# Optimization experiments

Measured on AMD Instinct MI355X. Metric: run time of the kernel, lower is better.

## Reference

```python
import jax, jax.numpy as jnp
import numpy as np

NUM_HEADS = 16


def setup_inputs() -> dict:
    key = jax.random.key(0)
    ks = jax.random.split(key, 6)
    B, S, D = 2, 2048, 1024
    x = jax.random.normal(ks[0], (B, S, D), dtype=jnp.float32)
    # Linear weights stored as [d_in, d_out] so forward is x @ W (qkv_bias=False)
    scale = 1.0 / np.sqrt(D)
    Wq = jax.random.normal(ks[1], (D, D), dtype=jnp.float32) * scale
    Wk = jax.random.normal(ks[2], (D, D), dtype=jnp.float32) * scale
    Wv = jax.random.normal(ks[3], (D, D), dtype=jnp.float32) * scale
    Wo = jax.random.normal(ks[4], (D, D), dtype=jnp.float32) * scale
    bo = jax.random.normal(ks[5], (D,), dtype=jnp.float32) * 0.01
    return {"x": x, "Wq": Wq, "Wk": Wk, "Wv": Wv, "Wo": Wo, "bo": bo}


def reference(x, Wq, Wk, Wv, Wo, bo):
    B, S, D = x.shape
    H = NUM_HEADS
    hd = D // H

    def split_heads(t):  # [B,S,D] -> [B,H,S,hd]
        return t.reshape(B, S, H, hd).transpose(0, 2, 1, 3)

    q = split_heads(x @ Wq)
    k = split_heads(x @ Wk)
    v = split_heads(x @ Wv)

    # full score matrix [B,H,S,S]
    scores = jnp.einsum('bhsd,bhtd->bhst', q, k)
    causal = jnp.triu(jnp.ones((S, S), dtype=bool), k=1)
    scores = jnp.where(causal, -jnp.inf, scores)
    attn = jax.nn.softmax(scores * (hd ** -0.5), axis=-1)
    # dropout p=0.0 -> identity
    out = jnp.einsum('bhst,bhtd->bhsd', attn, v)
    out = out.transpose(0, 2, 1, 3).reshape(B, S, D)
    return out @ Wo + bo
```

## Files before the change

### kernel.cpp

```cpp
#include <hip/hip_runtime.h>

typedef unsigned short ushort_t;
typedef unsigned int uint_t;
typedef __attribute__((ext_vector_type(8))) short short8;
typedef __attribute__((ext_vector_type(4))) float floatx4;

#define S_LEN 2048
#define D_DIM 1024
#define H_NUM 16
#define HD 64
#define GBUF (128 * 32)

__device__ __forceinline__ float bf2f(ushort_t u) {
    union { uint_t i; float f; } c; c.i = ((uint_t)u) << 16; return c.f;
}
__device__ __forceinline__ ushort_t f2bf(float f) {
    union { float f; uint_t i; } c; c.f = f;
    uint_t r = c.i + 0x7fffu + ((c.i >> 16) & 1u);
    return (ushort_t)(r >> 16);
}

__device__ __forceinline__ void g2l16(const ushort_t* g, ushort_t* l) {
    __builtin_amdgcn_global_load_lds(
        (const __attribute__((address_space(1))) void*)g,
        (__attribute__((address_space(3))) void*)l, 16, 0, 0);
}

__global__ __launch_bounds__(256, 4) void cast_x_kernel(
        const float* __restrict__ in, ushort_t* __restrict__ out) {
    const int idx = (blockIdx.x * 256 + threadIdx.x) * 4;
    const float4 v = *(const float4*)(in + idx);
    ushort4 o;
    o.x = f2bf(v.x); o.y = f2bf(v.y); o.z = f2bf(v.z); o.w = f2bf(v.w);
    *(ushort4*)(out + idx) = o;
}

__global__ __launch_bounds__(256, 2) void transpose4_kernel(
        const float* __restrict__ W0, const float* __restrict__ W1,
        const float* __restrict__ W2, const float* __restrict__ W3,
        ushort_t* __restrict__ T0, ushort_t* __restrict__ T1,
        ushort_t* __restrict__ T2, ushort_t* __restrict__ T3) {
    const int z = blockIdx.z;
    const float* in  = (z == 0) ? W0 : (z == 1) ? W1 : (z == 2) ? W2 : W3;
    ushort_t*    out = (z == 0) ? T0 : (z == 1) ? T1 : (z == 2) ? T2 : T3;
    __shared__ __align__(16) ushort_t t[64][65];
    const int r0 = blockIdx.y * 64, c0 = blockIdx.x * 64;
    const int tr = threadIdx.x >> 4;
    const int tc = (threadIdx.x & 15) * 4;
#pragma unroll
    for (int i = 0; i < 4; ++i) {
        const int row = tr + i * 16;
        const float4 v = *(const float4*)(in + (size_t)(r0 + row) * D_DIM + c0 + tc);
        t[row][tc + 0] = f2bf(v.x); t[row][tc + 1] = f2bf(v.y);
        t[row][tc + 2] = f2bf(v.z); t[row][tc + 3] = f2bf(v.w);
    }
    __syncthreads();
#pragma unroll
    for (int i = 0; i < 4; ++i) {
        const int n = tr + i * 16;
        ushort4 v;
        v.x = t[tc + 0][n]; v.y = t[tc + 1][n];
        v.z = t[tc + 2][n]; v.w = t[tc + 3][n];
        *(ushort4*)(out + (size_t)(c0 + n) * D_DIM + r0 + tc) = v;
    }
}

__device__ __forceinline__ void gemm_tile(
        const ushort_t* __restrict__ A, const ushort_t* __restrict__ BT,
        const int m0, const int n0,
        ushort_t* As, ushort_t* Bs, floatx4 acc[4][4]) {
    const int tid  = threadIdx.x;
    const int w    = tid >> 6;
    const int wm   = (w >> 1) * 64;
    const int wn   = (w & 1) * 64;
    const int lrow = tid & 15;
    const int kq   = ((tid & 63) >> 4) * 8;

    const int flat0 = tid * 8;
    const int flat1 = (256 + tid) * 8;
    const int row0 = flat0 >> 5, kk0 = flat0 & 31;
    const int row1 = flat1 >> 5, kk1 = flat1 & 31;

    const ushort_t* ga0 = A  + (size_t)(m0 + row0) * D_DIM + kk0;
    const ushort_t* gb0 = BT + (size_t)(n0 + row0) * D_DIM + kk0;
    const ushort_t* ga1 = A  + (size_t)(m0 + row1) * D_DIM + kk1;
    const ushort_t* gb1 = BT + (size_t)(n0 + row1) * D_DIM + kk1;

    g2l16(ga0, As + flat0);
    g2l16(gb0, Bs + flat0);
    g2l16(ga1, As + flat1);
    g2l16(gb1, Bs + flat1);
    asm volatile("s_waitcnt vmcnt(0)" ::: "memory");
    __syncthreads();

    int cur = 0;
    for (int k0 = 0; k0 < D_DIM; k0 += 32) {
        const ushort_t* Ac = As + cur * GBUF;
        const ushort_t* Bc = Bs + cur * GBUF;
        short8 av[4], bv[4];
#pragma unroll
        for (int i = 0; i < 4; ++i)
            av[i] = *(const short8*)(Ac + (wm + i * 16 + lrow) * 32 + kq);
#pragma unroll
        for (int j = 0; j < 4; ++j)
            bv[j] = *(const short8*)(Bc + (wn + j * 16 + lrow) * 32 + kq);

        if (k0 + 32 < D_DIM) {
            ushort_t* An = As + (cur ^ 1) * GBUF;
            ushort_t* Bn = Bs + (cur ^ 1) * GBUF;
            g2l16(ga0 + k0 + 32, An + flat0);
            g2l16(gb0 + k0 + 32, Bn + flat0);
            g2l16(ga1 + k0 + 32, An + flat1);
            g2l16(gb1 + k0 + 32, Bn + flat1);
        }

#pragma unroll
        for (int i = 0; i < 4; ++i)
#pragma unroll
            for (int j = 0; j < 4; ++j)
                acc[i][j] = __builtin_amdgcn_mfma_f32_16x16x32_bf16(
                    av[i], bv[j], acc[i][j], 0, 0, 0);

        asm volatile("s_waitcnt vmcnt(0)" ::: "memory");
        __syncthreads();
        cur ^= 1;
    }
}

__global__ __launch_bounds__(256, 2) void gemm_qkv_kernel(
        const ushort_t* __restrict__ A,
        const ushort_t* __restrict__ WqT, const ushort_t* __restrict__ WkT,
        const ushort_t* __restrict__ WvT,
        ushort_t* __restrict__ Qo, ushort_t* __restrict__ Ko,
        ushort_t* __restrict__ Vo) {
    const ushort_t* BT = (blockIdx.z == 0) ? WqT : (blockIdx.z == 1) ? WkT : WvT;
    ushort_t* C        = (blockIdx.z == 0) ? Qo  : (blockIdx.z == 1) ? Ko  : Vo;
    const float sc     = (blockIdx.z == 0) ? 0.125f : 1.0f;
    __shared__ __align__(16) ushort_t As[2 * GBUF];
    __shared__ __align__(16) ushort_t Bs[2 * GBUF];
    const int m0 = blockIdx.y * 128, n0 = blockIdx.x * 128;

    floatx4 acc[4][4] = {};
    gemm_tile(A, BT, m0, n0, As, Bs, acc);

    const int tid = threadIdx.x;
    const int w = tid >> 6, wm = (w >> 1) * 64, wn = (w & 1) * 64;
    const int lrow = tid & 15;
    const int rquad = ((tid & 63) >> 4) * 4;
#pragma unroll
    for (int i = 0; i < 4; ++i) {
        const int mbase = m0 + wm + i * 16 + rquad;
#pragma unroll
        for (int j = 0; j < 4; ++j) {
            const int gn = n0 + wn + j * 16 + lrow;
#pragma unroll
            for (int r = 0; r < 4; ++r)
                C[(size_t)(mbase + r) * D_DIM + gn] = f2bf(acc[i][j][r] * sc);
        }
    }
}

__global__ __launch_bounds__(256, 2) void gemm_out_kernel(
        const ushort_t* __restrict__ A, const ushort_t* __restrict__ WoT,
        const float* __restrict__ bias, float* __restrict__ C) {
    __shared__ __align__(16) ushort_t As[2 * GBUF];
    __shared__ __align__(16) ushort_t Bs[2 * GBUF];
    const int m0 = blockIdx.y * 128, n0 = blockIdx.x * 128;

    floatx4 acc[4][4] = {};
    gemm_tile(A, WoT, m0, n0, As, Bs, acc);

    const int tid = threadIdx.x;
    const int w = tid >> 6, wm = (w >> 1) * 64, wn = (w & 1) * 64;
    const int lrow = tid & 15;
    const int rquad = ((tid & 63) >> 4) * 4;
#pragma unroll
    for (int i = 0; i < 4; ++i) {
        const int mbase = m0 + wm + i * 16 + rquad;
#pragma unroll
        for (int j = 0; j < 4; ++j) {
            const int gn = n0 + wn + j * 16 + lrow;
            const float badd = bias[gn];
#pragma unroll
            for (int r = 0; r < 4; ++r)
                C[(size_t)(mbase + r) * D_DIM + gn] = acc[i][j][r] + badd;
        }
    }
}

__global__ __launch_bounds__(256, 4) void attn_mfma_kernel(
        const ushort_t* __restrict__ Q, const ushort_t* __restrict__ K,
        const ushort_t* __restrict__ V, ushort_t* __restrict__ O) {
    __shared__ __align__(16) ushort_t Ks[64 * 64];
    __shared__ __align__(16) ushort_t Vt[64 * 64];
    __shared__ __align__(16) ushort_t Ps[4][16 * 64];

    const int bh  = blockIdx.x;
    const int b   = bh >> 4, h = bh & 15;
    const int g   = blockIdx.y & 7;
    const int p   = blockIdx.y >> 3;
    const int qt  = (p == 0) ? g : (p == 1) ? (15 - g)
                  : (p == 2) ? (16 + g) : (31 - g);
    const int q0  = qt * 64;
    const int tid = threadIdx.x;
    const int wq  = tid >> 6;
    const int lane = tid & 63;
    const int col  = lane & 15;
    const int quad = lane >> 4;
    const int c7 = col & 7;
    const int qw0  = q0 + wq * 16;
    const size_t rowbase = (size_t)b * S_LEN;
    const int ch0 = h * HD;

    const int skey = tid >> 2;
    const int schk = tid & 3;
    const int vkp = tid & 31;
    const int vdc = tid >> 5;

    short8 aq[2];
#pragma unroll
    for (int kc = 0; kc < 2; ++kc)
        aq[kc] = *(const short8*)(Q + (rowbase + qw0 + col) * D_DIM
                                    + ch0 + kc * 32 + quad * 8);

    floatx4 oacc[4] = {};
    float mrun[4], lrun[4];
#pragma unroll
    for (int r = 0; r < 4; ++r) { mrun[r] = -1e30f; lrun[r] = 0.0f; }

    const int ntiles = qt + 1;

    short8 krA, krB, vrA, vrB;
    {
        const ushort_t* kg = K + (rowbase + skey) * D_DIM + ch0 + schk * 16;
        krA = *(const short8*)(kg);
        krB = *(const short8*)(kg + 8);
        const ushort_t* vg = V + (rowbase + 2 * vkp) * D_DIM + ch0 + vdc * 8;
        vrA = *(const short8*)(vg);
        vrB = *(const short8*)(vg + D_DIM);
    }

    for (int t = 0; t < ntiles; ++t) {
        const int kb = t * 64;
        __syncthreads();
        {
            const int sw = skey & 7;
            *(short8*)(Ks + skey * 64 + (((2 * schk) ^ sw) << 3)) = krA;
            *(short8*)(Ks + skey * 64 + (((2 * schk + 1) ^ sw) << 3)) = krB;
        }
#pragma unroll
        for (int e = 0; e < 8; ++e) {
            const int d = vdc * 8 + e;
            const uint_t pk = (uint_t)(ushort_t)vrA[e] | ((uint_t)(ushort_t)vrB[e] << 16);
            *(uint_t*)(Vt + d * 64 + ((2 * vkp) ^ ((d & 7) << 3))) = pk;
        }
        {
            const int kbn = (t + 1 < ntiles) ? (t + 1) * 64 : 0;
            const ushort_t* kg = K + (rowbase + kbn + skey) * D_DIM + ch0 + schk * 16;
            krA = *(const short8*)(kg);
            krB = *(const short8*)(kg + 8);
            const ushort_t* vg = V + (rowbase + kbn + 2 * vkp) * D_DIM + ch0 + vdc * 8;
            vrA = *(const short8*)(vg);
            vrB = *(const short8*)(vg + D_DIM);
        }
        __syncthreads();

        if (kb <= qw0 + 15) {
            floatx4 sa[4] = {};
            __builtin_amdgcn_s_setprio(1);
#pragma unroll
            for (int kc = 0; kc < 2; ++kc)
#pragma unroll
                for (int j = 0; j < 4; ++j) {
                    const short8 bk = *(const short8*)(
                        Ks + (j * 16 + col) * 64 + (((kc * 4 + quad) ^ c7) << 3));
                    sa[j] = __builtin_amdgcn_mfma_f32_16x16x32_bf16(
                        aq[kc], bk, sa[j], 0, 0, 0);
                }
            __builtin_amdgcn_s_setprio(0);

            const bool needmask = (kb + 63 > qw0);
            if (needmask) {
#pragma unroll
                for (int j = 0; j < 4; ++j)
#pragma unroll
                    for (int r = 0; r < 4; ++r) {
                        const int row = qw0 + quad * 4 + r;
                        const int key = kb + j * 16 + col;
                        if (key > row) sa[j][r] = -1e30f;
                    }
            }
#pragma unroll
            for (int r = 0; r < 4; ++r) {
                float mx = fmaxf(fmaxf(sa[0][r], sa[1][r]),
                                 fmaxf(sa[2][r], sa[3][r]));
                mx = fmaxf(mx, __shfl_xor(mx, 1));
                mx = fmaxf(mx, __shfl_xor(mx, 2));
                mx = fmaxf(mx, __shfl_xor(mx, 4));
                mx = fmaxf(mx, __shfl_xor(mx, 8));
                const float mn = fmaxf(mrun[r], mx);
                const float al = __expf(mrun[r] - mn);
                mrun[r] = mn;
                float rs = 0.0f;
#pragma unroll
                for (int j = 0; j < 4; ++j) {
                    const float p2 = __expf(sa[j][r] - mn);
                    sa[j][r] = p2;
                    rs += p2;
                }
                lrun[r] = lrun[r] * al + rs;
#pragma unroll
                for (int jd = 0; jd < 4; ++jd) oacc[jd][r] *= al;
            }
            {
                ushort_t* pw = Ps[wq];
#pragma unroll
                for (int j = 0; j < 4; ++j)
#pragma unroll
                    for (int r = 0; r < 4; ++r) {
                        const int row = quad * 4 + r;
                        pw[row * 64 + ((j * 16 + col) ^ ((row & 7) << 3))] =
                            f2bf(sa[j][r]);
                    }
            }
            asm volatile("s_waitcnt lgkmcnt(0)" ::: "memory");
            __builtin_amdgcn_s_setprio(1);
#pragma unroll
            for (int kc = 0; kc < 2; ++kc) {
                const short8 ap = *(const short8*)(
                    Ps[wq] + col * 64 + (((kc * 4 + quad) ^ c7) << 3));
#pragma unroll
                for (int jd = 0; jd < 4; ++jd) {
                    const short8 bv = *(const short8*)(
                        Vt + (jd * 16 + col) * 64 + (((kc * 4 + quad) ^ c7) << 3));
                    oacc[jd] = __builtin_amdgcn_mfma_f32_16x16x32_bf16(
                        ap, bv, oacc[jd], 0, 0, 0);
                }
            }
            __builtin_amdgcn_s_setprio(0);
        }
    }

#pragma unroll
    for (int r = 0; r < 4; ++r) {
        float l = lrun[r];
        l += __shfl_xor(l, 1);
        l += __shfl_xor(l, 2);
        l += __shfl_xor(l, 4);
        l += __shfl_xor(l, 8);
        const int row = qw0 + quad * 4 + r;
        const float inv = 1.0f / l;
#pragma unroll
        for (int jd = 0; jd < 4; ++jd)
            O[(rowbase + row) * D_DIM + ch0 + jd * 16 + col] =
                f2bf(oacc[jd][r] * inv);
    }
}

extern "C" void kernel_launch(void* const* d_in, const int* in_sizes, int n_in,
                              void* d_out, int out_size, void* d_ws, size_t ws_size,
                              hipStream_t stream) {
    const float* x  = (const float*)d_in[0];
    const float* Wq = (const float*)d_in[1];
    const float* Wk = (const float*)d_in[2];
    const float* Wv = (const float*)d_in[3];
    const float* Wo = (const float*)d_in[4];
    const float* bo = (const float*)d_in[5];
    float* out = (float*)d_out;

    char* ws = (char*)d_ws;
    const size_t MB = 1024 * 1024;
    ushort_t* xb  = (ushort_t*)(ws + 0 * MB);
    ushort_t* WqT = (ushort_t*)(ws + 8 * MB);
    ushort_t* WkT = (ushort_t*)(ws + 10 * MB);
    ushort_t* WvT = (ushort_t*)(ws + 12 * MB);
    ushort_t* WoT = (ushort_t*)(ws + 14 * MB);
    ushort_t* Qb  = (ushort_t*)(ws + 16 * MB);
    ushort_t* Kb  = (ushort_t*)(ws + 24 * MB);
    ushort_t* Vb  = (ushort_t*)(ws + 32 * MB);
    ushort_t* Ob  = (ushort_t*)(ws + 40 * MB);

    cast_x_kernel<<<4096, 256, 0, stream>>>(x, xb);
    transpose4_kernel<<<dim3(16, 16, 4), 256, 0, stream>>>(
        Wq, Wk, Wv, Wo, WqT, WkT, WvT, WoT);

    gemm_qkv_kernel<<<dim3(8, 32, 3), 256, 0, stream>>>(
        xb, WqT, WkT, WvT, Qb, Kb, Vb);

    attn_mfma_kernel<<<dim3(32, 32), 256, 0, stream>>>(Qb, Kb, Vb, Ob);

    gemm_out_kernel<<<dim3(8, 32), 256, 0, stream>>>(Ob, WoT, bo, out);
}
```

Measured before the change: 200.0 us.

## Narrow GEMM N-tile to 64, use exp2 softmax with lazy max rescaling

Both projection GEMMs move from 128x128 to 128x64 tiles, which doubles the grid and raises launch bounds to 4 blocks per SM so the 1024-wide outputs fill more of the GPU. The attention softmax folds log2(e) into the Q scale so it can use native exp2. It also skips the running-max rescale of the output accumulator unless a new row maximum exceeds the old one by a threshold. The smaller tiles reduce data reuse per block, and the lazy rescale lets exponentials grow up to about 2^11.5 before renormalising, which is a numerical-range risk.

After: 278.9 us. 39.4% more time.

```diff
diff --git a/kernel.cpp b/kernel.cpp
--- a/kernel.cpp
+++ b/kernel.cpp
@@ -9,7 +9,8 @@
 #define D_DIM 1024
 #define H_NUM 16
 #define HD 64
-#define GBUF (128 * 32)
+#define ABUF (128 * 32)
+#define BBUF (64 * 32)
 
 __device__ __forceinline__ float bf2f(ushort_t u) {
     union { uint_t i; float f; } c; c.i = ((uint_t)u) << 16; return c.f;
@@ -68,56 +69,54 @@
 __device__ __forceinline__ void gemm_tile(
         const ushort_t* __restrict__ A, const ushort_t* __restrict__ BT,
         const int m0, const int n0,
-        ushort_t* As, ushort_t* Bs, floatx4 acc[4][4]) {
+        ushort_t* As, ushort_t* Bs, floatx4 acc[4][2]) {
     const int tid  = threadIdx.x;
     const int w    = tid >> 6;
     const int wm   = (w >> 1) * 64;
-    const int wn   = (w & 1) * 64;
+    const int wn   = (w & 1) * 32;
     const int lrow = tid & 15;
     const int kq   = ((tid & 63) >> 4) * 8;
 
     const int flat0 = tid * 8;
     const int flat1 = (256 + tid) * 8;
-    const int row0 = flat0 >> 5, kk0 = flat0 & 31;
-    const int row1 = flat1 >> 5, kk1 = flat1 & 31;
-
-    const ushort_t* ga0 = A  + (size_t)(m0 + row0) * D_DIM + kk0;
-    const ushort_t* gb0 = BT + (size_t)(n0 + row0) * D_DIM + kk0;
-    const ushort_t* ga1 = A  + (size_t)(m0 + row1) * D_DIM + kk1;
-    const ushort_t* gb1 = BT + (size_t)(n0 + row1) * D_DIM + kk1;
+    const int rowA0 = flat0 >> 5, kkA0 = flat0 & 31;
+    const int rowA1 = flat1 >> 5, kkA1 = flat1 & 31;
+    const int rowB  = tid >> 2,  kkB  = (tid & 3) * 8;
+
+    const ushort_t* ga0 = A  + (size_t)(m0 + rowA0) * D_DIM + kkA0;
+    const ushort_t* ga1 = A  + (size_t)(m0 + rowA1) * D_DIM + kkA1;
+    const ushort_t* gb  = BT + (size_t)(n0 + rowB)  * D_DIM + kkB;
 
     g2l16(ga0, As + flat0);
-    g2l16(gb0, Bs + flat0);
     g2l16(ga1, As + flat1);
-    g2l16(gb1, Bs + flat1);
+    g2l16(gb,  Bs + tid * 8);
     asm volatile("s_waitcnt vmcnt(0)" ::: "memory");
     __syncthreads();
 
     int cur = 0;
     for (int k0 = 0; k0 < D_DIM; k0 += 32) {
-        const ushort_t* Ac = As + cur * GBUF;
-        const ushort_t* Bc = Bs + cur * GBUF;
-        short8 av[4], bv[4];
+        const ushort_t* Ac = As + cur * ABUF;
+        const ushort_t* Bc = Bs + cur * BBUF;
+        short8 av[4], bv[2];
 #pragma unroll
         for (int i = 0; i < 4; ++i)
             av[i] = *(const short8*)(Ac + (wm + i * 16 + lrow) * 32 + kq);
 #pragma unroll
-        for (int j = 0; j < 4; ++j)
+        for (int j = 0; j < 2; ++j)
             bv[j] = *(const short8*)(Bc + (wn + j * 16 + lrow) * 32 + kq);
 
         if (k0 + 32 < D_DIM) {
-            ushort_t* An = As + (cur ^ 1) * GBUF;
-            ushort_t* Bn = Bs + (cur ^ 1) * GBUF;
+            ushort_t* An = As + (cur ^ 1) * ABUF;
+            ushort_t* Bn = Bs + (cur ^ 1) * BBUF;
             g2l16(ga0 + k0 + 32, An + flat0);
-            g2l16(gb0 + k0 + 32, Bn + flat0);
             g2l16(ga1 + k0 + 32, An + flat1);
-            g2l16(gb1 + k0 + 32, Bn + flat1);
+            g2l16(gb  + k0 + 32, Bn + tid * 8);
         }
 
 #pragma unroll
         for (int i = 0; i < 4; ++i)
 #pragma unroll
-            for (int j = 0; j < 4; ++j)
+            for (int j = 0; j < 2; ++j)
                 acc[i][j] = __builtin_amdgcn_mfma_f32_16x16x32_bf16(
                     av[i], bv[j], acc[i][j], 0, 0, 0);
 
@@ -127,7 +126,7 @@
     }
 }
 
-__global__ __launch_bounds__(256, 2) void gemm_qkv_kernel(
+__global__ __launch_bounds__(256, 4) void gemm_qkv_kernel(
         const ushort_t* __restrict__ A,
         const ushort_t* __restrict__ WqT, const ushort_t* __restrict__ WkT,
         const ushort_t* __restrict__ WvT,
@@ -135,23 +134,23 @@
         ushort_t* __restrict__ Vo) {
     const ushort_t* BT = (blockIdx.z == 0) ? WqT : (blockIdx.z == 1) ? WkT : WvT;
     ushort_t* C        = (blockIdx.z == 0) ? Qo  : (blockIdx.z == 1) ? Ko  : Vo;
-    const float sc     = (blockIdx.z == 0) ? 0.125f : 1.0f;
-    __shared__ __align__(16) ushort_t As[2 * GBUF];
-    __shared__ __align__(16) ushort_t Bs[2 * GBUF];
-    const int m0 = blockIdx.y * 128, n0 = blockIdx.x * 128;
-
-    floatx4 acc[4][4] = {};
+    const float sc     = (blockIdx.z == 0) ? 0.18033688f : 1.0f;
+    __shared__ __align__(16) ushort_t As[2 * ABUF];
+    __shared__ __align__(16) ushort_t Bs[2 * BBUF];
+    const int m0 = blockIdx.y * 128, n0 = blockIdx.x * 64;
+
+    floatx4 acc[4][2] = {};
     gemm_tile(A, BT, m0, n0, As, Bs, acc);
 
     const int tid = threadIdx.x;
-    const int w = tid >> 6, wm = (w >> 1) * 64, wn = (w & 1) * 64;
+    const int w = tid >> 6, wm = (w >> 1) * 64, wn = (w & 1) * 32;
     const int lrow = tid & 15;
     const int rquad = ((tid & 63) >> 4) * 4;
 #pragma unroll
     for (int i = 0; i < 4; ++i) {
         const int mbase = m0 + wm + i * 16 + rquad;
 #pragma unroll
-        for (int j = 0; j < 4; ++j) {
+        for (int j = 0; j < 2; ++j) {
             const int gn = n0 + wn + j * 16 + lrow;
 #pragma unroll
             for (int r = 0; r < 4; ++r)
@@ -160,25 +159,25 @@
     }
 }
 
-__global__ __launch_bounds__(256, 2) void gemm_out_kernel(
+__global__ __launch_bounds__(256, 4) void gemm_out_kernel(
         const ushort_t* __restrict__ A, const ushort_t* __restrict__ WoT,
         const float* __restrict__ bias, float* __restrict__ C) {
-    __shared__ __align__(16) ushort_t As[2 * GBUF];
-    __shared__ __align__(16) ushort_t Bs[2 * GBUF];
-    const int m0 = blockIdx.y * 128, n0 = blockIdx.x * 128;
-
-    floatx4 acc[4][4] = {};
+    __shared__ __align__(16) ushort_t As[2 * ABUF];
+    __shared__ __align__(16) ushort_t Bs[2 * BBUF];
+    const int m0 = blockIdx.y * 128, n0 = blockIdx.x * 64;
+
+    floatx4 acc[4][2] = {};
     gemm_tile(A, WoT, m0, n0, As, Bs, acc);
 
     const int tid = threadIdx.x;
-    const int w = tid >> 6, wm = (w >> 1) * 64, wn = (w & 1) * 64;
+    const int w = tid >> 6, wm = (w >> 1) * 64, wn = (w & 1) * 32;
     const int lrow = tid & 15;
     const int rquad = ((tid & 63) >> 4) * 4;
 #pragma unroll
     for (int i = 0; i < 4; ++i) {
         const int mbase = m0 + wm + i * 16 + rquad;
 #pragma unroll
-        for (int j = 0; j < 4; ++j) {
+        for (int j = 0; j < 2; ++j) {
             const int gn = n0 + wn + j * 16 + lrow;
             const float badd = bias[gn];
 #pragma unroll
@@ -290,6 +289,7 @@
                         if (key > row) sa[j][r] = -1e30f;
                     }
             }
+            float mx4[4];
 #pragma unroll
             for (int r = 0; r < 4; ++r) {
                 float mx = fmaxf(fmaxf(sa[0][r], sa[1][r]),
@@ -298,19 +298,40 @@
                 mx = fmaxf(mx, __shfl_xor(mx, 2));
                 mx = fmaxf(mx, __shfl_xor(mx, 4));
                 mx = fmaxf(mx, __shfl_xor(mx, 8));
-                const float mn = fmaxf(mrun[r], mx);
-                const float al = __expf(mrun[r] - mn);
-                mrun[r] = mn;
-                float rs = 0.0f;
-#pragma unroll
-                for (int j = 0; j < 4; ++j) {
-                    const float p2 = __expf(sa[j][r] - mn);
-                    sa[j][r] = p2;
-                    rs += p2;
+                mx4[r] = mx;
+            }
+            bool grow = false;
+#pragma unroll
+            for (int r = 0; r < 4; ++r) grow |= (mx4[r] > mrun[r] + 11.5f);
+            if (__any(grow)) {
+#pragma unroll
+                for (int r = 0; r < 4; ++r) {
+                    const float mn = fmaxf(mrun[r], mx4[r]);
+                    const float al = __builtin_amdgcn_exp2f(mrun[r] - mn);
+                    mrun[r] = mn;
+                    float rs = 0.0f;
+#pragma unroll
+                    for (int j = 0; j < 4; ++j) {
+                        const float p2 = __builtin_amdgcn_exp2f(sa[j][r] - mn);
+                        sa[j][r] = p2;
+                        rs += p2;
+                    }
+                    lrun[r] = lrun[r] * al + rs;
+#pragma unroll
+                    for (int jd = 0; jd < 4; ++jd) oacc[jd][r] *= al;
                 }
-                lrun[r] = lrun[r] * al + rs;
-#pragma unroll
-                for (int jd = 0; jd < 4; ++jd) oacc[jd][r] *= al;
+            } else {
+#pragma unroll
+                for (int r = 0; r < 4; ++r) {
+                    float rs = 0.0f;
+#pragma unroll
+                    for (int j = 0; j < 4; ++j) {
+                        const float p2 = __builtin_amdgcn_exp2f(sa[j][r] - mrun[r]);
+                        sa[j][r] = p2;
+                        rs += p2;
+                    }
+                    lrun[r] += rs;
+                }
             }
             {
                 ushort_t* pw = Ps[wq];
@@ -384,10 +405,10 @@
     transpose4_kernel<<<dim3(16, 16, 4), 256, 0, stream>>>(
         Wq, Wk, Wv, Wo, WqT, WkT, WvT, WoT);
 
-    gemm_qkv_kernel<<<dim3(8, 32, 3), 256, 0, stream>>>(
+    gemm_qkv_kernel<<<dim3(16, 32, 3), 256, 0, stream>>>(
         xb, WqT, WkT, WvT, Qb, Kb, Vb);
 
     attn_mfma_kernel<<<dim3(32, 32), 256, 0, stream>>>(Qb, Kb, Vb, Ob);
 
-    gemm_out_kernel<<<dim3(8, 32), 256, 0, stream>>>(Ob, WoT, bo, out);
-}
+    gemm_out_kernel<<<dim3(16, 32), 256, 0, stream>>>(Ob, WoT, bo, out);
+}
```
